# Performance work log

Measured on AMD Instinct MI355X. Metric: run time of the kernel, lower is better.

The kernel has to match this reference:

```python
import jax, jax.numpy as jnp
import numpy as np

N = 100_000      # nodes
E = 1_600_000    # edges (avg degree 16)
D = 128          # emb_dim == hidden_dim
OUT = 128        # out_dim
NUM_BOND_TYPE = 6
NUM_BOND_DIR = 3


def _xavier(key, fan_in, fan_out, shape):
    a = np.sqrt(6.0 / (fan_in + fan_out)).astype(np.float32)
    return jax.random.uniform(key, shape, jnp.float32, -a, a)


def setup_inputs() -> dict:
    key = jax.random.key(0)
    ks = jax.random.split(key, 12)
    x = jax.random.normal(ks[0], (N, D), jnp.float32)
    edge_index = jax.random.randint(ks[1], (2, E), 0, N)
    edge_attr = jax.random.randint(ks[2], (E, 2), 0, NUM_BOND_DIR)
    # PReLU single learnable slope (torch init 0.25)
    prelu_a = jnp.full((1,), 0.25, jnp.float32)
    # enc_to_dec: Linear(D, D, bias=False), torch default uniform(-1/sqrt(D), 1/sqrt(D))
    s = 1.0 / np.sqrt(D)
    W_enc = jax.random.uniform(ks[3], (D, D), jnp.float32, -s, s)
    # edge embedding tables, xavier_uniform
    emb1 = _xavier(ks[4], NUM_BOND_TYPE, D, (NUM_BOND_TYPE, D))
    emb2 = _xavier(ks[5], NUM_BOND_DIR, D, (NUM_BOND_DIR, D))
    # GIN MLP: Linear(D, 2D) -> ReLU -> Linear(2D, OUT)
    W1 = jax.random.uniform(ks[6], (2 * D, D), jnp.float32, -s, s)
    b1 = jax.random.uniform(ks[7], (2 * D,), jnp.float32, -s, s)
    s2 = 1.0 / np.sqrt(2 * D)
    W2 = jax.random.uniform(ks[8], (OUT, 2 * D), jnp.float32, -s2, s2)
    b2 = jax.random.uniform(ks[9], (OUT,), jnp.float32, -s2, s2)
    return {
        "x": x, "edge_index": edge_index, "edge_attr": edge_attr,
        "prelu_a": prelu_a, "W_enc": W_enc,
        "emb1": emb1, "emb2": emb2,
        "W1": W1, "b1": b1, "W2": W2, "b2": b2,
    }


def reference(x, edge_index, edge_attr, prelu_a, W_enc, emb1, emb2, W1, b1, W2, b2):
    # PReLU then enc_to_dec (no bias)
    h = jnp.where(x >= 0, x, prelu_a * x)          # [N, D]
    h = h @ W_enc.T                                 # [N, D]
    src, dst = edge_index[0], edge_index[1]
    # edge embeddings for real edges
    e_emb = emb1[edge_attr[:, 0]] + emb2[edge_attr[:, 1]]  # [E, D]
    # messages: x_j + edge_attr, scatter-add at dst
    msg = h[src] + e_emb                             # [E, D]
    agg = jax.ops.segment_sum(msg, dst, num_segments=N)    # [N, D]
    # self-loops: appended edge (i, i) with attr [4, 0]
    self_emb = emb1[4] + emb2[0]                     # [D]
    agg = agg + h + self_emb[None, :]
    # GIN update MLP
    hid = jax.nn.relu(agg @ W1.T + b1)               # [N, 2D]
    out = hid @ W2.T + b2                            # [N, OUT]
    return out
```

## Files before the change

### kernel.cpp

```cpp
#include <hip/hip_runtime.h>
#include <hip/hip_bf16.h>

#define DD 128

typedef short bf16x8 __attribute__((ext_vector_type(8)));
typedef float f32x4 __attribute__((ext_vector_type(4)));

__device__ __forceinline__ float bf2f_lo(unsigned int u) {
    union { unsigned int v; float f; } x; x.v = u << 16; return x.f;
}
__device__ __forceinline__ float bf2f_hi(unsigned int u) {
    union { unsigned int v; float f; } x; x.v = u & 0xFFFF0000u; return x.f;
}
__device__ __forceinline__ unsigned short f2bf(float f) {
    union { float f; unsigned int u; } x; x.f = f;
    unsigned int u = x.u;
    unsigned int r = (u + 0x7FFFu + ((u >> 16) & 1u)) >> 16;
    return (unsigned short)r;
}

#define SBSH 7
#define SBN  128
#define NBP  256
#define NSBMAX 800
#define PKCAP 4096

__global__ __launch_bounds__(256) void sbwc_k(
    const int* __restrict__ ei, int* __restrict__ bh,
    const float* __restrict__ Wenc, const float* __restrict__ W1,
    const float* __restrict__ W2, unsigned short* __restrict__ wb,
    int E, int chunk, int nsb)
{
    __shared__ int h4[4][NSBMAX];
    const int b = blockIdx.x;
    if (b < NBP) {
        int wid = threadIdx.x >> 6;
        for (int i = threadIdx.x; i < 4 * NSBMAX; i += 256) ((int*)h4)[i] = 0;
        __syncthreads();
        int beg = b * chunk, end = min(E, beg + chunk);
        for (int e = beg + threadIdx.x; e < end; e += 256)
            atomicAdd(&h4[wid][ei[E + e] >> SBSH], 1);
        __syncthreads();
        for (int i = threadIdx.x; i < nsb; i += 256)
            bh[i * NBP + b] = h4[0][i] + h4[1][i] + h4[2][i] + h4[3][i];
        return;
    }
    int i = ((b - NBP) * 256 + threadIdx.x) * 4;
    if (i >= 81920) return;
    const float* src;
    int off;
    if (i < 16384)      { src = Wenc; off = 0; }
    else if (i < 49152) { src = W1;   off = 16384; }
    else                { src = W2;   off = 49152; }
    float4 v = *(const float4*)&src[i - off];
    ushort4 w;
    w.x = f2bf(v.x); w.y = f2bf(v.y); w.z = f2bf(v.z); w.w = f2bf(v.w);
    *(ushort4*)&wb[i] = w;
}

__global__ __launch_bounds__(256) void pscan1_k(const int* __restrict__ bh,
                                                int* __restrict__ bsum, int ntot) {
    __shared__ int ws[4];
    int base = blockIdx.x * 2048 + threadIdx.x * 8;
    int s = 0;
    #pragma unroll
    for (int i = 0; i < 8; ++i) { int idx = base + i; if (idx < ntot) s += bh[idx]; }
    int lane = threadIdx.x & 63, wid = threadIdx.x >> 6;
    int ss = s;
    #pragma unroll
    for (int o = 1; o < 64; o <<= 1) { int t = __shfl_up(ss, o, 64); if (lane >= o) ss += t; }
    if (lane == 63) ws[wid] = ss;
    __syncthreads();
    if (threadIdx.x == 0) bsum[blockIdx.x] = ws[0] + ws[1] + ws[2] + ws[3];
}

__global__ __launch_bounds__(256) void pscan3_k(const int* __restrict__ bh,
                                                const int* __restrict__ bsum,
                                                int* __restrict__ bho, int ntot) {
    __shared__ int ws[4];
    __shared__ int boff;
    const int b = blockIdx.x;
    const int t = threadIdx.x;
    const int lane = t & 63, wid = t >> 6;

    int pv = (t < b) ? bsum[t] : 0;
    #pragma unroll
    for (int o = 32; o; o >>= 1) pv += __shfl_xor(pv, o, 64);
    if (lane == 0) ws[wid] = pv;
    __syncthreads();
    if (t == 0) boff = ws[0] + ws[1] + ws[2] + ws[3];
    __syncthreads();

    int base = b * 2048 + t * 8;
    int v[8]; int s = 0;
    #pragma unroll
    for (int i = 0; i < 8; ++i) { int idx = base + i; v[i] = (idx < ntot) ? bh[idx] : 0; s += v[i]; }
    int ss = s;
    #pragma unroll
    for (int o = 1; o < 64; o <<= 1) { int u = __shfl_up(ss, o, 64); if (lane >= o) ss += u; }
    if (lane == 63) ws[wid] = ss;
    __syncthreads();
    if (t == 0) { int c = 0; for (int w = 0; w < 4; ++w) { int u = ws[w]; ws[w] = c; c += u; } }
    __syncthreads();
    int excl = ss - s + ws[wid] + boff;
    #pragma unroll
    for (int i = 0; i < 8; ++i) {
        int idx = base + i;
        if (idx < ntot) bho[idx] = excl;
        excl += v[i];
    }
}

__global__ __launch_bounds__(256) void pg_k(
    const int* __restrict__ ei, const int* __restrict__ ea,
    const int* __restrict__ bho, int* __restrict__ rec,
    const float* __restrict__ x, const unsigned short* __restrict__ Wb,
    unsigned short* __restrict__ Hb, const float* __restrict__ prelu_a,
    int E, int chunk, int nsb, int M)
{
    __shared__ int cur[NSBMAX];
    const int tid = threadIdx.x;

    if (blockIdx.x < NBP) {
        int b = blockIdx.x;
        for (int i = tid; i < nsb; i += 256) cur[i] = bho[i * NBP + b];
        __syncthreads();
        int beg = b * chunk, end = min(E, beg + chunk);
        for (int e = beg + tid; e < end; e += 256) {
            int src = ei[e];
            int dst = ei[E + e];
            int2 aa = *(const int2*)&ea[2 * e];
            int pos = atomicAdd(&cur[dst >> SBSH], 1);
            rec[pos] = src | ((aa.x * 3 + aa.y) << 17) | ((dst & (SBN - 1)) << 21);
        }
        return;
    }

    const int K = 128;
    const int wid = tid >> 6, lane = tid & 63;
    const float pa = prelu_a[0];
    const int r0 = (blockIdx.x - NBP) * 128 + wid * 32;
    const int rl = lane & 15, kb = (lane >> 4) * 8;

    bf16x8 af[2][4];
    #pragma unroll
    for (int rf = 0; rf < 2; ++rf) {
        int row = r0 + rf * 16 + rl; if (row > M - 1) row = M - 1;
        #pragma unroll
        for (int kf = 0; kf < 4; ++kf) {
            float4 v0 = *(const float4*)&x[(size_t)row * K + kf * 32 + kb];
            float4 v1 = *(const float4*)&x[(size_t)row * K + kf * 32 + kb + 4];
            v0.x = v0.x >= 0.f ? v0.x : pa * v0.x;
            v0.y = v0.y >= 0.f ? v0.y : pa * v0.y;
            v0.z = v0.z >= 0.f ? v0.z : pa * v0.z;
            v0.w = v0.w >= 0.f ? v0.w : pa * v0.w;
            v1.x = v1.x >= 0.f ? v1.x : pa * v1.x;
            v1.y = v1.y >= 0.f ? v1.y : pa * v1.y;
            v1.z = v1.z >= 0.f ? v1.z : pa * v1.z;
            v1.w = v1.w >= 0.f ? v1.w : pa * v1.w;
            bf16x8 t;
            t[0] = (short)f2bf(v0.x); t[1] = (short)f2bf(v0.y);
            t[2] = (short)f2bf(v0.z); t[3] = (short)f2bf(v0.w);
            t[4] = (short)f2bf(v1.x); t[5] = (short)f2bf(v1.y);
            t[6] = (short)f2bf(v1.z); t[7] = (short)f2bf(v1.w);
            af[rf][kf] = t;
        }
    }

    f32x4 acc[8][2];
    const f32x4 zz = {0.f, 0.f, 0.f, 0.f};
    #pragma unroll
    for (int nt = 0; nt < 8; ++nt) { acc[nt][0] = zz; acc[nt][1] = zz; }

    #pragma unroll
    for (int nt = 0; nt < 8; ++nt) {
        bf16x8 bf[4];
        #pragma unroll
        for (int kf = 0; kf < 4; ++kf)
            bf[kf] = *(const bf16x8*)&Wb[(size_t)(nt * 16 + rl) * K + kf * 32 + kb];
        #pragma unroll
        for (int rf = 0; rf < 2; ++rf)
            #pragma unroll
            for (int kf = 0; kf < 4; ++kf)
                acc[nt][rf] = __builtin_amdgcn_mfma_f32_16x16x32_bf16(af[rf][kf], bf[kf], acc[nt][rf], 0, 0, 0);
    }

    const int rq = (lane >> 4) * 4;
    #pragma unroll
    for (int nt = 0; nt < 8; ++nt) {
        int c = nt * 16 + rl;
        #pragma unroll
        for (int rf = 0; rf < 2; ++rf) {
            int rb = r0 + rf * 16 + rq;
            #pragma unroll
            for (int t = 0; t < 4; ++t) {
                int r = rb + t;
                if (r < M) Hb[(size_t)r * 128 + c] = f2bf(acc[nt][rf][t]);
            }
        }
    }
}

__global__ __launch_bounds__(1024) void csragg_k(
    const unsigned short* __restrict__ h,
    const int* __restrict__ rec,
    const int* __restrict__ bho,
    const float* __restrict__ emb1, const float* __restrict__ emb2,
    int* __restrict__ packed, unsigned int* __restrict__ aggb,
    int nsb, int M, int E)
{
    __shared__ float emb12[10][DD];
    __shared__ int hist[SBN];
    __shared__ int lstart[SBN];
    __shared__ int wsum[2];
    __shared__ int pkl[PKCAP];
    const int s = blockIdx.x;
    const int t = threadIdx.x;
    const int lane = t & 63, wid = t >> 6;

    for (int i = t; i < 10 * DD; i += 1024) {
        int c = i >> 7, col = i & 127;
        float v;
        if (c == 9) v = emb1[4 * DD + col] + emb2[col];
        else        v = emb1[(c / 3) * DD + col] + emb2[(c % 3) * DD + col];
        emb12[c][col] = v;
    }
    int sb0 = bho[s * NBP];
    int sb1 = (s == nsb - 1) ? E : bho[(s + 1) * NBP];
    if (t < SBN) hist[t] = 0;
    __syncthreads();

    const bool inlds = (sb1 - sb0) <= PKCAP;

    for (int i = sb0 + t; i < sb1; i += 1024)
        atomicAdd(&hist[(rec[i] >> 21) & (SBN - 1)], 1);
    __syncthreads();

    int v = (t < SBN) ? hist[t] : 0;
    int ss = v;
    #pragma unroll
    for (int o = 1; o < 64; o <<= 1) { int u = __shfl_up(ss, o, 64); if (lane >= o) ss += u; }
    if (t < SBN && lane == 63) wsum[wid] = ss;
    __syncthreads();
    if (t == 0) { int c = 0; for (int w = 0; w < 2; ++w) { int x2 = wsum[w]; wsum[w] = c; c += x2; } }
    __syncthreads();
    if (t < SBN) {
        lstart[t] = ss - v + wsum[wid];
        hist[t] = 0;
    }
    __syncthreads();

    if (inlds) {
        for (int i = sb0 + t; i < sb1; i += 1024) {
            int r = rec[i];
            int dl = (r >> 21) & (SBN - 1);
            int pos = lstart[dl] + atomicAdd(&hist[dl], 1);
            pkl[pos] = r & 0x1FFFFF;
        }
    } else {
        for (int i = sb0 + t; i < sb1; i += 1024) {
            int r = rec[i];
            int dl = (r >> 21) & (SBN - 1);
            int pos = sb0 + lstart[dl] + atomicAdd(&hist[dl], 1);
            packed[pos] = r & 0x1FFFFF;
        }
    }
    __syncthreads();

    const int n0 = s << SBSH;
    const int c2 = lane * 2;
    #pragma unroll
    for (int k = 0; k < SBN / 16; ++k) {
        int r = wid + k * 16;
        int n = n0 + r;
        if (n >= M) continue;
        int lbeg = lstart[r];
        int lend = lbeg + hist[r];
        unsigned int hn = *(const unsigned int*)&h[(size_t)n * DD + c2];
        float2 acc = {bf2f_lo(hn) + emb12[9][c2], bf2f_hi(hn) + emb12[9][c2 + 1]};
        if (inlds) {
            int e = lbeg;
            for (; e + 8 <= lend; e += 8) {
                int p[8]; unsigned int hv[8]; float2 m[8];
                #pragma unroll
                for (int i = 0; i < 8; ++i) p[i] = pkl[e + i];
                #pragma unroll
                for (int i = 0; i < 8; ++i)
                    hv[i] = *(const unsigned int*)&h[(size_t)(p[i] & 0x1FFFF) * DD + c2];
                #pragma unroll
                for (int i = 0; i < 8; ++i)
                    m[i] = *(const float2*)&emb12[(p[i] >> 17) & 15][c2];
                #pragma unroll
                for (int i = 0; i < 8; ++i) {
                    acc.x += bf2f_lo(hv[i]) + m[i].x;
                    acc.y += bf2f_hi(hv[i]) + m[i].y;
                }
            }
            for (; e < lend; ++e) {
                int p = pkl[e];
                unsigned int hv = *(const unsigned int*)&h[(size_t)(p & 0x1FFFF) * DD + c2];
                float2 m = *(const float2*)&emb12[(p >> 17) & 15][c2];
                acc.x += bf2f_lo(hv) + m.x;
                acc.y += bf2f_hi(hv) + m.y;
            }
        } else {
            int e = sb0 + lbeg, end = sb0 + lend;
            for (; e + 8 <= end; e += 8) {
                int p[8]; unsigned int hv[8]; float2 m[8];
                #pragma unroll
                for (int i = 0; i < 8; ++i) p[i] = packed[e + i];
                #pragma unroll
                for (int i = 0; i < 8; ++i)
                    hv[i] = *(const unsigned int*)&h[(size_t)(p[i] & 0x1FFFF) * DD + c2];
                #pragma unroll
                for (int i = 0; i < 8; ++i)
                    m[i] = *(const float2*)&emb12[(p[i] >> 17) & 15][c2];
                #pragma unroll
                for (int i = 0; i < 8; ++i) {
                    acc.x += bf2f_lo(hv[i]) + m[i].x;
                    acc.y += bf2f_hi(hv[i]) + m[i].y;
                }
            }
            for (; e < end; ++e) {
                int p = packed[e];
                unsigned int hv = *(const unsigned int*)&h[(size_t)(p & 0x1FFFF) * DD + c2];
                float2 m = *(const float2*)&emb12[(p >> 17) & 15][c2];
                acc.x += bf2f_lo(hv) + m.x;
                acc.y += bf2f_hi(hv) + m.y;
            }
        }
        aggb[((size_t)n * DD + c2) >> 1] = ((unsigned int)f2bf(acc.y) << 16) | f2bf(acc.x);
    }
}

__global__ __launch_bounds__(1024) void mlp_k(
    const unsigned short* __restrict__ A,
    const unsigned short* __restrict__ w1b,
    const float* __restrict__ b1,
    const unsigned short* __restrict__ w2b,
    const float* __restrict__ b2,
    float* __restrict__ out, int M)
{
    __shared__ unsigned short W1l[256][136];
    __shared__ unsigned short hidl[128][264];
    unsigned short (*W2l)[264] = (unsigned short (*)[264])&W1l[0][0];

    const int tid = threadIdx.x;
    const int wid = tid >> 6, lane = tid & 63;
    const int rl = lane & 15, kb = (lane >> 4) * 8;
    const int rq = (lane >> 4) * 4;
    const int rf = wid & 7, ch = wid >> 3;
    const int r0 = blockIdx.x * 128;

    for (int idx = tid; idx < 256 * 16; idx += 1024) {
        int n = idx >> 4, kq = idx & 15;
        *(ushort4*)&W1l[n][kq * 8] = *(const ushort4*)&w1b[(size_t)n * 128 + kq * 8];
        *(ushort4*)&W1l[n][kq * 8 + 4] = *(const ushort4*)&w1b[(size_t)n * 128 + kq * 8 + 4];
    }
    bf16x8 af[4];
    {
        int row = r0 + rf * 16 + rl; if (row > M - 1) row = M - 1;
        #pragma unroll
        for (int kf = 0; kf < 4; ++kf)
            af[kf] = *(const bf16x8*)&A[(size_t)row * 128 + kf * 32 + kb];
    }
    __syncthreads();

    f32x4 acc1[8];
    const f32x4 zz = {0.f, 0.f, 0.f, 0.f};
    #pragma unroll
    for (int j = 0; j < 8; ++j) acc1[j] = zz;
    #pragma unroll
    for (int j = 0; j < 8; ++j) {
        int nt = ch * 8 + j;
        bf16x8 bf[4];
        #pragma unroll
        for (int kf = 0; kf < 4; ++kf)
            bf[kf] = *(const bf16x8*)&W1l[nt * 16 + rl][kf * 32 + kb];
        #pragma unroll
        for (int kf = 0; kf < 4; ++kf)
            acc1[j] = __builtin_amdgcn_mfma_f32_16x16x32_bf16(af[kf], bf[kf], acc1[j], 0, 0, 0);
    }
    #pragma unroll
    for (int j = 0; j < 8; ++j) {
        int c = (ch * 8 + j) * 16 + rl;
        float bi = b1[c];
        #pragma unroll
        for (int tt = 0; tt < 4; ++tt)
            hidl[rf * 16 + rq + tt][c] = f2bf(fmaxf(acc1[j][tt] + bi, 0.f));
    }
    __syncthreads();

    for (int idx = tid; idx < 128 * 32; idx += 1024) {
        int n = idx >> 5, kq = idx & 31;
        *(ushort4*)&W2l[n][kq * 8] = *(const ushort4*)&w2b[(size_t)n * 256 + kq * 8];
        *(ushort4*)&W2l[n][kq * 8 + 4] = *(const ushort4*)&w2b[(size_t)n * 256 + kq * 8 + 4];
    }
    bf16x8 af2[8];
    #pragma unroll
    for (int kf = 0; kf < 8; ++kf)
        af2[kf] = *(const bf16x8*)&hidl[rf * 16 + rl][kf * 32 + kb];
    __syncthreads();

    f32x4 acc2[4];
    #pragma unroll
    for (int j = 0; j < 4; ++j) acc2[j] = zz;
    #pragma unroll
    for (int j = 0; j < 4; ++j) {
        int nt = ch * 4 + j;
        bf16x8 bf[8];
        #pragma unroll
        for (int kf = 0; kf < 8; ++kf)
            bf[kf] = *(const bf16x8*)&W2l[nt * 16 + rl][kf * 32 + kb];
        #pragma unroll
        for (int kf = 0; kf < 8; ++kf)
            acc2[j] = __builtin_amdgcn_mfma_f32_16x16x32_bf16(af2[kf], bf[kf], acc2[j], 0, 0, 0);
    }
    #pragma unroll
    for (int j = 0; j < 4; ++j) {
        int c = (ch * 4 + j) * 16 + rl;
        float bi = b2[c];
        #pragma unroll
        for (int tt = 0; tt < 4; ++tt) {
            int r = r0 + rf * 16 + rq + tt;
            if (r < M) out[(size_t)r * 128 + c] = acc2[j][tt] + bi;
        }
    }
}

extern "C" void kernel_launch(void* const* d_in, const int* in_sizes, int n_in,
                              void* d_out, int out_size, void* d_ws, size_t ws_size,
                              hipStream_t stream) {
    const float* x     = (const float*)d_in[0];
    const int*   ei    = (const int*)d_in[1];
    const int*   ea    = (const int*)d_in[2];
    const float* pa    = (const float*)d_in[3];
    const float* Wenc  = (const float*)d_in[4];
    const float* emb1  = (const float*)d_in[5];
    const float* emb2  = (const float*)d_in[6];
    const float* W1    = (const float*)d_in[7];
    const float* b1    = (const float*)d_in[8];
    const float* W2    = (const float*)d_in[9];
    const float* b2    = (const float*)d_in[10];
    float* out = (float*)d_out;

    const int M = in_sizes[0] / DD;
    const int E = in_sizes[1] / 2;
    const int nsb = (M + SBN - 1) >> SBSH;
    const int chunk = (E + NBP - 1) / NBP;
    const int ntot = nsb * NBP;
    const int nscb = (ntot + 2047) / 2048;

    char* ws = (char*)d_ws;
    size_t o = 0;
    unsigned short* h_bf  = (unsigned short*)(ws + o); o += (size_t)M * DD * 2;
    unsigned int*   aggb  = (unsigned int*)(ws + o);   o += (size_t)M * DD * 2;
    int* rec    = (int*)(ws + o); o += (size_t)E * 4;
    int* packed = (int*)(ws + o); o += (size_t)E * 4;
    int* bh     = (int*)(ws + o); o += (size_t)ntot * 4;
    int* bho    = (int*)(ws + o); o += (size_t)ntot * 4;
    int* bsum   = (int*)(ws + o); o += (size_t)nscb * 4;
    unsigned short* wb = (unsigned short*)(ws + o); o += 81920 * 2;
    unsigned short* wenc_b = wb;
    unsigned short* w1_b   = wb + 16384;
    unsigned short* w2_b   = wb + 49152;

    const int gm = (M + 127) / 128;
    dim3 blk(256);

    sbwc_k<<<dim3(NBP + 80), blk, 0, stream>>>(ei, bh, Wenc, W1, W2, wb, E, chunk, nsb);

    pscan1_k<<<dim3(nscb), blk, 0, stream>>>(bh, bsum, ntot);
    pscan3_k<<<dim3(nscb), blk, 0, stream>>>(bh, bsum, bho, ntot);

    pg_k<<<dim3(NBP + gm), blk, 0, stream>>>(
        ei, ea, bho, rec, x, wenc_b, h_bf, pa, E, chunk, nsb, M);

    csragg_k<<<dim3(nsb), dim3(1024), 0, stream>>>(
        h_bf, rec, bho, emb1, emb2, packed, aggb, nsb, M, E);

    mlp_k<<<dim3(gm), dim3(1024), 0, stream>>>(
        (const unsigned short*)aggb, w1_b, b1, w2_b, b2, out, M);
}
```

Measured before the change: 182.9 us.

## Make MLP kernel persistent with weights resident in LDS over 32-row tiles

The MLP kernel now runs as a persistent grid capped at 256 blocks. Each block loads W1 and W2 into separate LDS buffers once, then loops over 32-row tiles instead of one 128-row tile per block. This removes the repeated per-block weight staging into shared memory across roughly 782 blocks. The cost is less work per wave per tile (fewer MFMAs between barriers), two barriers per tile, and LDS use of about 136KB, which limits occupancy to one block per CU.

Result: no change. 185.1 us (+1.2%).

```diff
diff --git a/kernel.cpp b/kernel.cpp
--- a/kernel.cpp
+++ b/kernel.cpp
@@ -339,92 +339,87 @@
     const float* __restrict__ b1,
     const unsigned short* __restrict__ w2b,
     const float* __restrict__ b2,
-    float* __restrict__ out, int M)
+    float* __restrict__ out, int M, int ntiles)
 {
     __shared__ unsigned short W1l[256][136];
-    __shared__ unsigned short hidl[128][264];
-    unsigned short (*W2l)[264] = (unsigned short (*)[264])&W1l[0][0];
+    __shared__ unsigned short W2l[128][264];
+    __shared__ unsigned short hidl[32][264];
 
     const int tid = threadIdx.x;
     const int wid = tid >> 6, lane = tid & 63;
     const int rl = lane & 15, kb = (lane >> 4) * 8;
     const int rq = (lane >> 4) * 4;
-    const int rf = wid & 7, ch = wid >> 3;
-    const int r0 = blockIdx.x * 128;
+    const int rf = wid & 1;
+    const int cw = wid >> 1;
 
     for (int idx = tid; idx < 256 * 16; idx += 1024) {
         int n = idx >> 4, kq = idx & 15;
-        *(ushort4*)&W1l[n][kq * 8] = *(const ushort4*)&w1b[(size_t)n * 128 + kq * 8];
+        *(ushort4*)&W1l[n][kq * 8]     = *(const ushort4*)&w1b[(size_t)n * 128 + kq * 8];
         *(ushort4*)&W1l[n][kq * 8 + 4] = *(const ushort4*)&w1b[(size_t)n * 128 + kq * 8 + 4];
     }
-    bf16x8 af[4];
-    {
-        int row = r0 + rf * 16 + rl; if (row > M - 1) row = M - 1;
-        #pragma unroll
-        for (int kf = 0; kf < 4; ++kf)
-            af[kf] = *(const bf16x8*)&A[(size_t)row * 128 + kf * 32 + kb];
-    }
-    __syncthreads();
-
-    f32x4 acc1[8];
-    const f32x4 zz = {0.f, 0.f, 0.f, 0.f};
-    #pragma unroll
-    for (int j = 0; j < 8; ++j) acc1[j] = zz;
-    #pragma unroll
-    for (int j = 0; j < 8; ++j) {
-        int nt = ch * 8 + j;
-        bf16x8 bf[4];
-        #pragma unroll
-        for (int kf = 0; kf < 4; ++kf)
-            bf[kf] = *(const bf16x8*)&W1l[nt * 16 + rl][kf * 32 + kb];
-        #pragma unroll
-        for (int kf = 0; kf < 4; ++kf)
-            acc1[j] = __builtin_amdgcn_mfma_f32_16x16x32_bf16(af[kf], bf[kf], acc1[j], 0, 0, 0);
-    }
-    #pragma unroll
-    for (int j = 0; j < 8; ++j) {
-        int c = (ch * 8 + j) * 16 + rl;
-        float bi = b1[c];
-        #pragma unroll
-        for (int tt = 0; tt < 4; ++tt)
-            hidl[rf * 16 + rq + tt][c] = f2bf(fmaxf(acc1[j][tt] + bi, 0.f));
-    }
-    __syncthreads();
-
     for (int idx = tid; idx < 128 * 32; idx += 1024) {
         int n = idx >> 5, kq = idx & 31;
-        *(ushort4*)&W2l[n][kq * 8] = *(const ushort4*)&w2b[(size_t)n * 256 + kq * 8];
+        *(ushort4*)&W2l[n][kq * 8]     = *(const ushort4*)&w2b[(size_t)n * 256 + kq * 8];
         *(ushort4*)&W2l[n][kq * 8 + 4] = *(const ushort4*)&w2b[(size_t)n * 256 + kq * 8 + 4];
     }
-    bf16x8 af2[8];
-    #pragma unroll
-    for (int kf = 0; kf < 8; ++kf)
-        af2[kf] = *(const bf16x8*)&hidl[rf * 16 + rl][kf * 32 + kb];
-    __syncthreads();
-
-    f32x4 acc2[4];
-    #pragma unroll
-    for (int j = 0; j < 4; ++j) acc2[j] = zz;
-    #pragma unroll
-    for (int j = 0; j < 4; ++j) {
-        int nt = ch * 4 + j;
-        bf16x8 bf[8];
+    __syncthreads();
+
+    const f32x4 zz = {0.f, 0.f, 0.f, 0.f};
+    for (int tile = blockIdx.x; tile < ntiles; tile += gridDim.x) {
+        const int r0 = tile * 32;
+        bf16x8 af[4];
+        {
+            int row = r0 + rf * 16 + rl; if (row > M - 1) row = M - 1;
+            #pragma unroll
+            for (int kf = 0; kf < 4; ++kf)
+                af[kf] = *(const bf16x8*)&A[(size_t)row * 128 + kf * 32 + kb];
+        }
+        f32x4 acc1[2] = {zz, zz};
+        #pragma unroll
+        for (int j = 0; j < 2; ++j) {
+            int nt = cw * 2 + j;
+            bf16x8 bf[4];
+            #pragma unroll
+            for (int kf = 0; kf < 4; ++kf)
+                bf[kf] = *(const bf16x8*)&W1l[nt * 16 + rl][kf * 32 + kb];
+            #pragma unroll
+            for (int kf = 0; kf < 4; ++kf)
+                acc1[j] = __builtin_amdgcn_mfma_f32_16x16x32_bf16(af[kf], bf[kf], acc1[j], 0, 0, 0);
+        }
+        #pragma unroll
+        for (int j = 0; j < 2; ++j) {
+            int c = (cw * 2 + j) * 16 + rl;
+            float bi = b1[c];
+            #pragma unroll
+            for (int tt = 0; tt < 4; ++tt)
+                hidl[rf * 16 + rq + tt][c] = f2bf(fmaxf(acc1[j][tt] + bi, 0.f));
+        }
+        __syncthreads();
+
+        bf16x8 af2[8];
         #pragma unroll
         for (int kf = 0; kf < 8; ++kf)
-            bf[kf] = *(const bf16x8*)&W2l[nt * 16 + rl][kf * 32 + kb];
-        #pragma unroll
-        for (int kf = 0; kf < 8; ++kf)
-            acc2[j] = __builtin_amdgcn_mfma_f32_16x16x32_bf16(af2[kf], bf[kf], acc2[j], 0, 0, 0);
-    }
-    #pragma unroll
-    for (int j = 0; j < 4; ++j) {
-        int c = (ch * 4 + j) * 16 + rl;
-        float bi = b2[c];
-        #pragma unroll
-        for (int tt = 0; tt < 4; ++tt) {
-            int r = r0 + rf * 16 + rq + tt;
-            if (r < M) out[(size_t)r * 128 + c] = acc2[j][tt] + bi;
-        }
+            af2[kf] = *(const bf16x8*)&hidl[rf * 16 + rl][kf * 32 + kb];
+        f32x4 acc2 = zz;
+        {
+            bf16x8 bf[8];
+            #pragma unroll
+            for (int kf = 0; kf < 8; ++kf)
+                bf[kf] = *(const bf16x8*)&W2l[cw * 16 + rl][kf * 32 + kb];
+            #pragma unroll
+            for (int kf = 0; kf < 8; ++kf)
+                acc2 = __builtin_amdgcn_mfma_f32_16x16x32_bf16(af2[kf], bf[kf], acc2, 0, 0, 0);
+        }
+        {
+            int c = cw * 16 + rl;
+            float bi = b2[c];
+            #pragma unroll
+            for (int tt = 0; tt < 4; ++tt) {
+                int r = r0 + rf * 16 + rq + tt;
+                if (r < M) out[(size_t)r * 128 + c] = acc2[tt] + bi;
+            }
+        }
+        __syncthreads();
     }
 }
 
@@ -450,6 +445,7 @@
     const int chunk = (E + NBP - 1) / NBP;
     const int ntot = nsb * NBP;
     const int nscb = (ntot + 2047) / 2048;
+    const int ntiles = (M + 31) / 32;
 
     char* ws = (char*)d_ws;
     size_t o = 0;
@@ -479,6 +475,7 @@
     csragg_k<<<dim3(nsb), dim3(1024), 0, stream>>>(
         h_bf, rec, bho, emb1, emb2, packed, aggb, nsb, M, E);
 
-    mlp_k<<<dim3(gm), dim3(1024), 0, stream>>>(
-        (const unsigned short*)aggb, w1_b, b1, w2_b, b2, out, M);
-}
+    int mgrid = ntiles < 256 ? ntiles : 256;
+    mlp_k<<<dim3(mgrid), dim3(1024), 0, stream>>>(
+        (const unsigned short*)aggb, w1_b, b1, w2_b, b2, out, M, ntiles);
+}
```
